# Optimization experiments

Hardware: AMD Instinct MI355X
Metric: run time of the kernel (lower is better)

Reference implementation:

```python
import jax, jax.numpy as jnp
import numpy as np

HIDDEN = 1024
BATCH, SEQ = 4, 2048

def setup_inputs() -> dict:
    key = jax.random.key(0)
    kx, kq, kk, kv, ko = jax.random.split(key, 5)
    s = 1.0 / np.sqrt(HIDDEN)
    return {
        "x": jax.random.normal(kx, (BATCH, SEQ, HIDDEN), dtype=jnp.float32),
        "Wq": jax.random.normal(kq, (HIDDEN, HIDDEN), dtype=jnp.float32) * s,
        "Wk": jax.random.normal(kk, (HIDDEN, HIDDEN), dtype=jnp.float32) * s,
        "Wv": jax.random.normal(kv, (HIDDEN, HIDDEN), dtype=jnp.float32) * s,
        "Wo": jax.random.normal(ko, (HIDDEN, HIDDEN), dtype=jnp.float32) * s,
    }

def reference(x, Wq, Wk, Wv, Wo):
    # torch Linear: y = x @ W.T; weights here stored as [out, in]
    q = jnp.einsum('bsd,ed->bse', x, Wq)
    k = jnp.einsum('bsd,ed->bse', x, Wk)
    v = jnp.einsum('bsd,ed->bse', x, Wv)
    score = jnp.einsum('bqe,bke->bqk', q, k)  # unscaled, per source
    score = jax.nn.softmax(score, axis=-1)
    out = jnp.einsum('bqk,bke->bqe', score, v)
    return jnp.einsum('bse,fe->bsf', out, Wo)
```

## Files before the change

kernel.cpp:

```cpp
#include <hip/hip_runtime.h>
#include <stdint.h>


typedef _Float16 f16_t;
typedef _Float16 f16x8 __attribute__((ext_vector_type(8)));
typedef _Float16 f16x4 __attribute__((ext_vector_type(4)));
typedef float    f32x4 __attribute__((ext_vector_type(4)));
typedef uint32_t u32;

__device__ __forceinline__ void gld_lds16(const void* g, void* l) {
    __builtin_amdgcn_global_load_lds(
        (const __attribute__((address_space(1))) void*)g,
        (__attribute__((address_space(3))) void*)l, 16, 0, 0);
}

__device__ __forceinline__ f16x8 ld128(const void* p) {
    f16x8 r;
    const u32 a = (u32)(uintptr_t)(__attribute__((address_space(3))) const void*)p;
    asm volatile("ds_read_b128 %0, %1" : "=v"(r) : "v"(a));
    return r;
}

template<int EPI>
__global__ __launch_bounds__(512, 2)
void gemm256(const f16_t* __restrict__ A0, const f16_t* __restrict__ A1,
             const f16_t* __restrict__ A2,
             const f16_t* __restrict__ B0, const f16_t* __restrict__ B1,
             const f16_t* __restrict__ B2,
             int NK, int lda, int ldb, long sA, long sB, long sC,
             void* __restrict__ C0v, int ldc,
             int nbx, int plane)
{
    __shared__ __align__(1024) char smem[131072];

    const int nwg = (int)gridDim.x;
    int id = (int)blockIdx.x;
    id = (id & 7) * (nwg >> 3) + (id >> 3);
    const int bz  = id / plane;
    const int rem = id - bz * plane;
    const int by  = rem / nbx;
    const int bx  = rem - by * nbx;
    const long bm = (long)by * 256;
    const long bn = (long)bx * 256;
    const long zA = (long)bz * sA, zB = (long)bz * sB;

    const int tid  = threadIdx.x;
    const int lane = tid & 63;
    const int wid  = tid >> 6;
    const int wr   = wid >> 2;
    const int wc   = wid & 3;
    const int fr   = lane & 15;
    const int kg   = lane >> 4;

    const int srow = tid >> 3;
    const int scol = ((tid & 7) ^ ((tid >> 4) & 6)) << 3;
    const int ldsw = wid << 10;

    const int swzb    = (fr & 12) << 3;
    const int koff[2] = { (kg * 16) ^ swzb, (64 + kg * 16) ^ swzb };
    const int aBase   = wr * 16384 + fr * 128;
    const int bBase   = 32768 + (wc >> 1) * 16384 + (wc & 1) * 8192 + fr * 128;

    f32x4 acc[8][4] = {};
    f16x8 bfr[4][2];

    auto stage = [&](int kt, int part, int buf) {
        const int seg    = kt >> 4;
        const int klocal = (kt & 15) << 6;
        const bool isB = part < 2;
        const f16_t* base;
        if (isB) base = (seg == 0) ? B0 : (seg == 1 ? B1 : B2);
        else     base = (seg == 0) ? A0 : (seg == 1 ? A1 : A2);
        const long rowb = (isB ? (bn + part * 128) : (bm + (part - 2) * 128)) + srow;
        const long zoff = isB ? zB : zA;
        const int  ld   = isB ? ldb : lda;
        const int  poff = isB ? (32768 + part * 16384) : ((part - 2) * 16384);
        #pragma unroll
        for (int c = 0; c < 2; ++c) {
            const f16_t* g = base + zoff + (rowb + c * 64) * (long)ld + klocal + scol;
            gld_lds16(g, smem + buf * 65536 + poff + c * 8192 + ldsw);
        }
    };

    #pragma unroll
    for (int ht = 0; ht < 7; ++ht) stage(ht >> 2, ht & 3, (ht >> 2) & 1);
    asm volatile("s_waitcnt vmcnt(6)" ::: "memory");
    __builtin_amdgcn_s_barrier();

    const int NI = NK >> 1;
    #pragma unroll 1
    for (int i = 0; i < NI; ++i) {
        const bool last = (i == NI - 1);
        #pragma unroll
        for (int p = 0; p < 8; ++p) {
            const int q  = p & 3;
            const int cb = (p >> 2) * 65536;
            if (q == 0) {
                #pragma unroll
                for (int fn = 0; fn < 4; ++fn)
                    #pragma unroll
                    for (int kh = 0; kh < 2; ++kh)
                        bfr[fn][kh] = ld128(smem + cb + bBase
                                            + fn * 2048 + koff[kh]);
            }
            f16x8 afr[2][2];
            #pragma unroll
            for (int m2 = 0; m2 < 2; ++m2)
                #pragma unroll
                for (int kh = 0; kh < 2; ++kh)
                    afr[m2][kh] = ld128(smem + cb + aBase
                                        + (q * 2 + m2) * 2048 + koff[kh]);
            const int sc = (7 + p) >> 2;
            if (p == 0 || !last) stage(2 * i + sc, (7 + p) & 3, sc & 1);
            __builtin_amdgcn_sched_barrier(0);
            __builtin_amdgcn_s_barrier();
            asm volatile("s_waitcnt lgkmcnt(0)" ::: "memory");
            __builtin_amdgcn_sched_barrier(0);
            __builtin_amdgcn_s_setprio(1);
            #pragma unroll
            for (int m2 = 0; m2 < 2; ++m2)
                #pragma unroll
                for (int fn = 0; fn < 4; ++fn)
                    #pragma unroll
                    for (int kh = 0; kh < 2; ++kh)
                        acc[q * 2 + m2][fn] = __builtin_amdgcn_mfma_f32_16x16x32_f16(
                            afr[m2][kh], bfr[fn][kh], acc[q * 2 + m2][fn], 0, 0, 0);
            __builtin_amdgcn_s_setprio(0);
            __builtin_amdgcn_sched_barrier(0);
            if (q == 3) {
                if (last) asm volatile("s_waitcnt vmcnt(0)" ::: "memory");
                else      asm volatile("s_waitcnt vmcnt(6)" ::: "memory");
            }
            __builtin_amdgcn_s_barrier();
        }
    }

    const int rq = kg * 4;
    #pragma unroll
    for (int m = 0; m < 8; ++m) {
        #pragma unroll
        for (int fn = 0; fn < 4; ++fn) {
            const long col = bn + wc * 64 + fn * 16 + fr;
            #pragma unroll
            for (int r = 0; r < 4; ++r) {
                const long row = bm + wr * 128 + m * 16 + rq + r;
                const float v = acc[m][fn][r];
                if constexpr (EPI == 0) {
                    ((float*)C0v)[(long)bz * sC + row * ldc + col] = v;
                } else {
                    const long off = (col >= 1024)
                        ? 8388608L + row * 1024 + (col - 1024)
                        : row * 1024 + col;
                    ((f16_t*)C0v)[off] = (f16_t)v;
                }
            }
        }
    }
}

#define BM 128
#define BN 128
#define BK 32

template<int EPI>
__global__ __launch_bounds__(256, 2)
void gemm_nt(const f16_t* __restrict__ A, const f16_t* __restrict__ B,
             int K, int lda, int ldb, long sA, long sB, long sC,
             void* __restrict__ C0v, int ldc, int nbx, int nby)
{
    __shared__ f16_t As[BM * BK];
    __shared__ f16_t Bs[BN * BK];

    const int nwg = (int)gridDim.x;
    int id = (int)blockIdx.x;
    id = (id & 7) * (nwg >> 3) + (id >> 3);
    const int plane = nbx * nby;
    const int bz  = id / plane;
    const int rem = id - bz * plane;
    const int by  = rem / nbx;
    const int bx  = rem - by * nbx;

    const long bm = (long)by * BM;
    const long bn = (long)bx * BN;

    const f16_t* A0 = A + (long)bz * sA;
    const f16_t* B0 = B + (long)bz * sB;

    const int tid  = threadIdx.x;
    const int lane = tid & 63;
    const int wid  = tid >> 6;
    const int wr   = wid >> 1;
    const int wc   = wid & 1;

    const int srow = tid >> 2;
    const int sgc  = (((tid & 3) ^ (srow & 3)) << 3);
    const int ldsb = wid * 512;

    const int fr  = lane & 15;
    const int kgs = (((lane >> 4) ^ (lane & 3)) << 3);

    f32x4 acc[4][4] = {};

    const long arow = (bm + srow) * (long)lda;
    const long brow = (bn + srow) * (long)ldb;

    for (int k0 = 0; k0 < K; k0 += BK) {
        const f16_t* a = A0 + arow + k0 + sgc;
        const f16_t* b = B0 + brow + k0 + sgc;
        gld_lds16(a,             &As[ldsb]);
        gld_lds16(a + 64L * lda, &As[2048 + ldsb]);
        gld_lds16(b,             &Bs[ldsb]);
        gld_lds16(b + 64L * ldb, &Bs[2048 + ldsb]);
        __syncthreads();

        f16x8 af[4], bg[4];
        #pragma unroll
        for (int m = 0; m < 4; ++m)
            af[m] = *(const f16x8*)&As[(wr * 64 + m * 16 + fr) * BK + kgs];
        #pragma unroll
        for (int n = 0; n < 4; ++n)
            bg[n] = *(const f16x8*)&Bs[(wc * 64 + n * 16 + fr) * BK + kgs];
        #pragma unroll
        for (int m = 0; m < 4; ++m)
            #pragma unroll
            for (int n = 0; n < 4; ++n)
                acc[m][n] = __builtin_amdgcn_mfma_f32_16x16x32_f16(
                    af[m], bg[n], acc[m][n], 0, 0, 0);
        __syncthreads();
    }

    const int rq = (lane >> 4) * 4;
    #pragma unroll
    for (int m = 0; m < 4; ++m) {
        #pragma unroll
        for (int n = 0; n < 4; ++n) {
            const long col = bn + wc * 64 + n * 16 + fr;
            #pragma unroll
            for (int r = 0; r < 4; ++r) {
                const long row = bm + wr * 64 + m * 16 + rq + r;
                const long idx = (long)bz * sC + row * ldc + col;
                const float v = acc[m][n][r];
                if constexpr (EPI == 0) ((float*)C0v)[idx] = v;
                else                    ((f16_t*)C0v)[idx] = (f16_t)v;
            }
        }
    }
}

template<bool SPLIT>
__global__ __launch_bounds__(256)
void cvt_f32_f16(const float* __restrict__ X, f16_t* __restrict__ Hh,
                 f16_t* __restrict__ Ll, int n)
{
    const int i = (blockIdx.x * 256 + threadIdx.x) * 4;
    if (i >= n) return;
    const f32x4 v = *(const f32x4*)&X[i];
    f16x4 h, l;
    #pragma unroll
    for (int j = 0; j < 4; ++j) {
        h[j] = (f16_t)v[j];
        if constexpr (SPLIT) l[j] = (f16_t)(v[j] - (float)h[j]);
    }
    *(f16x4*)&Hh[i] = h;
    if constexpr (SPLIT) *(f16x4*)&Ll[i] = l;
}

__global__ __launch_bounds__(256)
void softmax_rows(const float* __restrict__ Sc, f16_t* __restrict__ P)
{
    constexpr int NC = 2048;
    const int row = blockIdx.x;
    const int tid = threadIdx.x;
    const float* s = Sc + (size_t)row * NC;

    float v[8];
    *(f32x4*)&v[0] = *(const f32x4*)&s[tid * 8];
    *(f32x4*)&v[4] = *(const f32x4*)&s[tid * 8 + 4];

    float m = v[0];
    #pragma unroll
    for (int j = 1; j < 8; ++j) m = fmaxf(m, v[j]);
    #pragma unroll
    for (int off = 1; off < 64; off <<= 1) m = fmaxf(m, __shfl_xor(m, off));

    __shared__ float redm[4], reds[4];
    if ((tid & 63) == 0) redm[tid >> 6] = m;
    __syncthreads();
    m = fmaxf(fmaxf(redm[0], redm[1]), fmaxf(redm[2], redm[3]));

    float sum = 0.f;
    #pragma unroll
    for (int j = 0; j < 8; ++j) { v[j] = __expf(v[j] - m); sum += v[j]; }
    #pragma unroll
    for (int off = 1; off < 64; off <<= 1) sum += __shfl_xor(sum, off);
    if ((tid & 63) == 0) reds[tid >> 6] = sum;
    __syncthreads();
    sum = reds[0] + reds[1] + reds[2] + reds[3];

    const float inv = 1.0f / sum;
    f16x8 o;
    #pragma unroll
    for (int j = 0; j < 8; ++j) o[j] = (f16_t)(v[j] * inv);
    *(f16x8*)(P + (size_t)row * NC + tid * 8) = o;
}

extern "C" void kernel_launch(void* const* d_in, const int* in_sizes, int n_in,
                              void* d_out, int out_size, void* d_ws, size_t ws_size,
                              hipStream_t stream)
{
    const float* x  = (const float*)d_in[0];
    const float* Wq = (const float*)d_in[1];
    const float* Wk = (const float*)d_in[2];
    const float* Wv = (const float*)d_in[3];
    const float* Wo = (const float*)d_in[4];
    float* out = (float*)d_out;

    constexpr long H = 1024, S = 2048, B = 4, NT = B * S;
    constexpr long HH = H * H;

    char* ws = (char*)d_ws;
    const size_t MB = 1u << 20;
    f16_t* xh    = (f16_t*)(ws + 0);
    float* score = (float*)(ws + 0);
    f16_t* wqk   = (f16_t*)(ws + 64 * MB);
    f16_t* wv    = (f16_t*)(ws + 68 * MB);
    f16_t* wo    = (f16_t*)(ws + 70 * MB);
    f16_t* qh    = (f16_t*)(ws + 72 * MB);
    f16_t* kh    = (f16_t*)(ws + 88 * MB);
    f16_t* attn  = (f16_t*)(ws + 72 * MB);
    f16_t* vT    = (f16_t*)(ws + 104 * MB);
    f16_t* xl    = (f16_t*)(ws + 120 * MB);
    f16_t* P     = (f16_t*)(ws + 120 * MB);

    const dim3 blk(256);

    cvt_f32_f16<true ><<<NT * H / 1024, blk, 0, stream>>>(x,  xh, xl, NT * H);
    cvt_f32_f16<false><<<HH / 1024, blk, 0, stream>>>(Wq, wqk,      nullptr, HH);
    cvt_f32_f16<false><<<HH / 1024, blk, 0, stream>>>(Wk, wqk + HH, nullptr, HH);
    cvt_f32_f16<false><<<HH / 1024, blk, 0, stream>>>(Wv, wv, nullptr, HH);
    cvt_f32_f16<false><<<HH / 1024, blk, 0, stream>>>(Wo, wo, nullptr, HH);

    gemm256<3><<<dim3(256), dim3(512), 0, stream>>>(
        xh, xl, xh, wqk, wqk, wqk, 32, (int)H, (int)H, 0L, 0L, 0L,
        qh, (int)H, 8, 256);

    gemm_nt<1><<<dim3(512), blk, 0, stream>>>(
        wv, xh, (int)H, (int)H, (int)H, 0L, 0L, 0L, vT, (int)NT, 64, 8);

    gemm256<0><<<dim3(256), dim3(512), 0, stream>>>(
        qh, qh, qh, kh, kh, kh, 16, (int)H, (int)H,
        S * H, S * H, S * S, score, (int)S, 8, 64);

    softmax_rows<<<dim3(B * S), blk, 0, stream>>>(score, P);

    gemm_nt<1><<<dim3(512), blk, 0, stream>>>(
        P, vT, (int)S, (int)S, (int)NT, S * S, S, S * H, attn, (int)H, 8, 16);

    gemm_nt<0><<<dim3(512), blk, 0, stream>>>(
        attn, wo, (int)H, (int)H, (int)H, 0L, 0L, 0L, out, (int)H, 8, 64);
}
```

Baseline: 251.8 us.

## Fold Wo into V projection and fuse input conversions into one prep kernel

Uses associativity, (P·V)·Woᵀ = P·(x·(Wo·Wv)ᵀ), to precompute Wvo = Wo·Wv as a small 1024³ GEMM. The V projection then uses Wvo directly and the final output projection GEMM over all tokens is removed. The five separate f32→f16 conversion launches become one prep kernel, which also transposes Wv through shared memory. The cost is an extra small GEMM and an added fp16 rounding of the combined weight, which may change accuracy.

```diff
diff --git a/kernel.cpp b/kernel.cpp
--- a/kernel.cpp
+++ b/kernel.cpp
@@ -247,22 +247,56 @@
     }
 }
 
-template<bool SPLIT>
 __global__ __launch_bounds__(256)
-void cvt_f32_f16(const float* __restrict__ X, f16_t* __restrict__ Hh,
-                 f16_t* __restrict__ Ll, int n)
-{
-    const int i = (blockIdx.x * 256 + threadIdx.x) * 4;
-    if (i >= n) return;
-    const f32x4 v = *(const f32x4*)&X[i];
-    f16x4 h, l;
-    #pragma unroll
-    for (int j = 0; j < 4; ++j) {
-        h[j] = (f16_t)v[j];
-        if constexpr (SPLIT) l[j] = (f16_t)(v[j] - (float)h[j]);
-    }
-    *(f16x4*)&Hh[i] = h;
-    if constexpr (SPLIT) *(f16x4*)&Ll[i] = l;
+void prep(const float* __restrict__ x,  const float* __restrict__ Wq,
+          const float* __restrict__ Wk, const float* __restrict__ Wo,
+          const float* __restrict__ Wv,
+          f16_t* __restrict__ xh, f16_t* __restrict__ xl,
+          f16_t* __restrict__ wqk, f16_t* __restrict__ wo16,
+          f16_t* __restrict__ wvT)
+{
+    const int bid = blockIdx.x;
+    const int tid = threadIdx.x;
+    if (bid < 8192) {
+        const int i = (bid * 256 + tid) * 4;
+        const f32x4 v = *(const f32x4*)&x[i];
+        f16x4 h, l;
+        #pragma unroll
+        for (int j = 0; j < 4; ++j) {
+            h[j] = (f16_t)v[j];
+            l[j] = (f16_t)(v[j] - (float)h[j]);
+        }
+        *(f16x4*)&xh[i] = h;
+        *(f16x4*)&xl[i] = l;
+    } else if (bid < 11264) {
+        const float* src; f16_t* dst;
+        if      (bid < 9216)  { src = Wq; dst = wqk;              }
+        else if (bid < 10240) { src = Wk; dst = wqk + 1024 * 1024; }
+        else                  { src = Wo; dst = wo16;             }
+        const int lb = (bid < 9216) ? bid - 8192 : (bid < 10240 ? bid - 9216 : bid - 10240);
+        const int i = (lb * 256 + tid) * 4;
+        const f32x4 v = *(const f32x4*)&src[i];
+        f16x4 h;
+        #pragma unroll
+        for (int j = 0; j < 4; ++j) h[j] = (f16_t)v[j];
+        *(f16x4*)&dst[i] = h;
+    } else {
+        __shared__ float tile[64][65];
+        const int b  = bid - 11264;
+        const int br = b >> 4, bc = b & 15;
+        const int c  = tid & 63;
+        #pragma unroll
+        for (int j = 0; j < 16; ++j) {
+            const int r = j * 4 + (tid >> 6);
+            tile[r][c] = Wv[(br * 64 + r) * 1024 + bc * 64 + c];
+        }
+        __syncthreads();
+        #pragma unroll
+        for (int j = 0; j < 16; ++j) {
+            const int r = j * 4 + (tid >> 6);
+            wvT[(bc * 64 + r) * 1024 + br * 64 + c] = (f16_t)tile[c][r];
+        }
+    }
 }
 
 __global__ __launch_bounds__(256)
@@ -316,46 +350,40 @@
     float* out = (float*)d_out;
 
     constexpr long H = 1024, S = 2048, B = 4, NT = B * S;
-    constexpr long HH = H * H;
 
     char* ws = (char*)d_ws;
     const size_t MB = 1u << 20;
     f16_t* xh    = (f16_t*)(ws + 0);
     float* score = (float*)(ws + 0);
     f16_t* wqk   = (f16_t*)(ws + 64 * MB);
-    f16_t* wv    = (f16_t*)(ws + 68 * MB);
-    f16_t* wo    = (f16_t*)(ws + 70 * MB);
-    f16_t* qh    = (f16_t*)(ws + 72 * MB);
-    f16_t* kh    = (f16_t*)(ws + 88 * MB);
-    f16_t* attn  = (f16_t*)(ws + 72 * MB);
-    f16_t* vT    = (f16_t*)(ws + 104 * MB);
-    f16_t* xl    = (f16_t*)(ws + 120 * MB);
-    f16_t* P     = (f16_t*)(ws + 120 * MB);
-
-    const dim3 blk(256);
-
-    cvt_f32_f16<true ><<<NT * H / 1024, blk, 0, stream>>>(x,  xh, xl, NT * H);
-    cvt_f32_f16<false><<<HH / 1024, blk, 0, stream>>>(Wq, wqk,      nullptr, HH);
-    cvt_f32_f16<false><<<HH / 1024, blk, 0, stream>>>(Wk, wqk + HH, nullptr, HH);
-    cvt_f32_f16<false><<<HH / 1024, blk, 0, stream>>>(Wv, wv, nullptr, HH);
-    cvt_f32_f16<false><<<HH / 1024, blk, 0, stream>>>(Wo, wo, nullptr, HH);
+    f16_t* wo16  = (f16_t*)(ws + 68 * MB);
+    f16_t* wvT   = (f16_t*)(ws + 70 * MB);
+    f16_t* wvo   = (f16_t*)(ws + 72 * MB);
+    f16_t* qh    = (f16_t*)(ws + 80 * MB);
+    f16_t* kh    = (f16_t*)(ws + 96 * MB);
+    f16_t* P     = (f16_t*)(ws + 80 * MB);
+    f16_t* uT    = (f16_t*)(ws + 112 * MB);
+    f16_t* xl    = (f16_t*)(ws + 128 * MB);
+
+    prep<<<dim3(11520), dim3(256), 0, stream>>>(x, Wq, Wk, Wo, Wv,
+                                                xh, xl, wqk, wo16, wvT);
 
     gemm256<3><<<dim3(256), dim3(512), 0, stream>>>(
         xh, xl, xh, wqk, wqk, wqk, 32, (int)H, (int)H, 0L, 0L, 0L,
         qh, (int)H, 8, 256);
 
-    gemm_nt<1><<<dim3(512), blk, 0, stream>>>(
-        wv, xh, (int)H, (int)H, (int)H, 0L, 0L, 0L, vT, (int)NT, 64, 8);
+    gemm_nt<1><<<dim3(64), dim3(256), 0, stream>>>(
+        wo16, wvT, (int)H, (int)H, (int)H, 0L, 0L, 0L, wvo, (int)H, 8, 8);
+
+    gemm_nt<1><<<dim3(512), dim3(256), 0, stream>>>(
+        wvo, xh, (int)H, (int)H, (int)H, 0L, 0L, 0L, uT, (int)NT, 64, 8);
 
     gemm256<0><<<dim3(256), dim3(512), 0, stream>>>(
         qh, qh, qh, kh, kh, kh, 16, (int)H, (int)H,
         S * H, S * H, S * S, score, (int)S, 8, 64);
 
-    softmax_rows<<<dim3(B * S), blk, 0, stream>>>(score, P);
-
-    gemm_nt<1><<<dim3(512), blk, 0, stream>>>(
-        P, vT, (int)S, (int)S, (int)NT, S * S, S, S * H, attn, (int)H, 8, 16);
-
-    gemm_nt<0><<<dim3(512), blk, 0, stream>>>(
-        attn, wo, (int)H, (int)H, (int)H, 0L, 0L, 0L, out, (int)H, 8, 64);
-}
+    softmax_rows<<<dim3(B * S), dim3(256), 0, stream>>>(score, P);
+
+    gemm_nt<0><<<dim3(512), dim3(256), 0, stream>>>(
+        P, uT, (int)S, (int)S, (int)NT, S * S, S, S * H, out, (int)H, 8, 16);
+}
```

New measurement: 242.5 us. 3.7% less time.
